# Kernel tuning notes

Hardware: AMD Instinct MI355X
Metric: run time of the kernel (lower is better)

Reference implementation:

```python
import jax, jax.numpy as jnp
import numpy as np

B, S, D, H = 2, 2048, 768, 12
DK = D // H


def setup_inputs() -> dict:
    key = jax.random.key(0)
    ks = jax.random.split(key, 12)
    inp = {
        "q": jax.random.normal(ks[0], (B, S, D), jnp.float32),
        "k": jax.random.normal(ks[1], (B, S, D), jnp.float32),
        "v": jax.random.normal(ks[2], (B, S, D), jnp.float32),
        # float mask: 1.0 where attention is disallowed (causal upper triangle)
        "mask": (1.0 - jnp.tril(jnp.ones((S, S), jnp.float32)))[None, None],
        "Wq": jax.random.normal(ks[3], (D, D), jnp.float32) / np.sqrt(D),
        "bq": jnp.zeros((D,), jnp.float32),
        "Wk": jax.random.normal(ks[4], (D, D), jnp.float32) / np.sqrt(D),
        "bk": jnp.zeros((D,), jnp.float32),
        "Wv": jax.random.normal(ks[5], (D, D), jnp.float32) / np.sqrt(D),
        "bv": jnp.zeros((D,), jnp.float32),
        "Wo": jax.random.normal(ks[6], (D, D), jnp.float32) / np.sqrt(D),
        "bo": jnp.zeros((D,), jnp.float32),
    }
    return inp


def _split_heads(x):
    # [B,S,D] -> [B,H,S,DK]
    b, s, _ = x.shape
    return x.reshape(b, s, H, DK).transpose(0, 2, 1, 3)


def reference(q, k, v, mask, Wq, bq, Wk, bk, Wv, bv, Wo, bo):
    Q = _split_heads(q @ Wq + bq)
    K = _split_heads(k @ Wk + bk)
    V = _split_heads(v @ Wv + bv)
    scale = jax.lax.rsqrt(jnp.float32(D))  # note: d_model, not d_k (faithful)
    logits = jnp.einsum("bhqd,bhkd->bhqk", Q, K) * scale
    logits = logits + (-1e9) * mask
    weights = jax.nn.softmax(logits, axis=-1)
    attn = jnp.einsum("bhqk,bhkd->bhqd", weights, V)
    attn = attn.transpose(0, 2, 1, 3).reshape(q.shape)  # [B,S,D]
    return jax.nn.relu(attn @ Wo + bo)
```

## Files before the change

### kernel.cpp

```cpp
#include <hip/hip_runtime.h>
#include <math.h>

#define BB 2
#define SS 2048
#define DD 768
#define HH 12
#define DKK 64
#define MM (BB*SS)

typedef _Float16 half_t;
using half8 = __attribute__((ext_vector_type(8))) _Float16;
using half4 = __attribute__((ext_vector_type(4))) _Float16;
using floatx4 = __attribute__((ext_vector_type(4))) float;

__global__ __launch_bounds__(256)
void prep(const float* __restrict__ q, const float* __restrict__ k,
          const float* __restrict__ v,
          const float* __restrict__ Wq, const float* __restrict__ Wk,
          const float* __restrict__ Wv, const float* __restrict__ Wo,
          half_t* __restrict__ qh, half_t* __restrict__ kh,
          half_t* __restrict__ vh,
          half_t* __restrict__ Wqt, half_t* __restrict__ Wkt,
          half_t* __restrict__ Wvt, half_t* __restrict__ Wot)
{
    __shared__ float tile[64][68];
    const int y = blockIdx.y;
    const int t = threadIdx.x;
    if (y < 3) {
        const float* src = y == 0 ? q : (y == 1 ? k : v);
        half_t* dst      = y == 0 ? qh : (y == 1 ? kh : vh);
        int i = blockIdx.x * 256 + t;
        float4 f = ((const float4*)src)[i];
        half4 hv;
        hv[0] = (half_t)f.x; hv[1] = (half_t)f.y;
        hv[2] = (half_t)f.z; hv[3] = (half_t)f.w;
        ((half4*)dst)[i] = hv;
    } else {
        int x = blockIdx.x;
        if (x >= 576) return;
        int w = x / 144, rem = x % 144;
        const float* W = w == 0 ? Wq : w == 1 ? Wk : w == 2 ? Wv : Wo;
        half_t* T      = w == 0 ? Wqt : w == 1 ? Wkt : w == 2 ? Wvt : Wot;
        int k0 = (rem % 12) * 64, n0 = (rem / 12) * 64;
        #pragma unroll
        for (int i = 0; i < 4; ++i) {
            int c = t + i * 256;
            int kr = c >> 4, nc = (c & 15) * 4;
            *(float4*)&tile[kr][nc] = *(const float4*)&W[(size_t)(k0 + kr) * DD + n0 + nc];
        }
        __syncthreads();
        #pragma unroll
        for (int i = 0; i < 4; ++i) {
            int c = t + i * 256;
            int nr = c >> 4, kc = (c & 15) * 4;
            half4 hv;
            #pragma unroll
            for (int jj = 0; jj < 4; ++jj) hv[jj] = (half_t)tile[kc + jj][nr];
            *(half4*)&T[(size_t)(n0 + nr) * DD + k0 + kc] = hv;
        }
    }
}

template<bool SWAP>
__device__ __forceinline__
void gemm_body(const half_t* __restrict__ A, const half_t* __restrict__ Bt,
               floatx4 (&acc)[4][2], half_t (*As)[72], half_t (*Bs)[72],
               int m0, int n0)
{
    const int t = threadIdx.x;
    const int lane = t & 63, wave = t >> 6;
    const int lr = lane & 15, lq = lane >> 4;
    const int wm = (wave >> 1) * 64, wn = (wave & 1) * 32;
    const int a_r = t >> 1,  a_c = (t & 1) * 32;
    const int b_r = t >> 2,  b_c = (t & 3) * 16;

    #pragma unroll
    for (int mi = 0; mi < 4; ++mi)
        #pragma unroll
        for (int ni = 0; ni < 2; ++ni)
            #pragma unroll
            for (int r = 0; r < 4; ++r) acc[mi][ni][r] = 0.f;

    for (int k0 = 0; k0 < DD; k0 += 64) {
        __syncthreads();
        #pragma unroll
        for (int jj = 0; jj < 4; ++jj)
            *(half8*)&As[a_r][a_c + jj * 8] =
                *(const half8*)&A[(size_t)(m0 + a_r) * DD + k0 + a_c + jj * 8];
        #pragma unroll
        for (int jj = 0; jj < 2; ++jj)
            *(half8*)&Bs[b_r][b_c + jj * 8] =
                *(const half8*)&Bt[(size_t)(n0 + b_r) * DD + k0 + b_c + jj * 8];
        __syncthreads();

        half8 af[4][2], bf[2][2];
        #pragma unroll
        for (int mi = 0; mi < 4; ++mi)
            #pragma unroll
            for (int kp = 0; kp < 2; ++kp)
                af[mi][kp] = *(const half8*)&As[wm + mi * 16 + lr][kp * 32 + lq * 8];
        #pragma unroll
        for (int ni = 0; ni < 2; ++ni)
            #pragma unroll
            for (int kp = 0; kp < 2; ++kp)
                bf[ni][kp] = *(const half8*)&Bs[wn + ni * 16 + lr][kp * 32 + lq * 8];

        #pragma unroll
        for (int mi = 0; mi < 4; ++mi)
            #pragma unroll
            for (int ni = 0; ni < 2; ++ni)
                #pragma unroll
                for (int kp = 0; kp < 2; ++kp) {
                    if (SWAP)
                        acc[mi][ni] = __builtin_amdgcn_mfma_f32_16x16x32_f16(
                            bf[ni][kp], af[mi][kp], acc[mi][ni], 0, 0, 0);
                    else
                        acc[mi][ni] = __builtin_amdgcn_mfma_f32_16x16x32_f16(
                            af[mi][kp], bf[ni][kp], acc[mi][ni], 0, 0, 0);
                }
    }
}

__global__ __launch_bounds__(256)
void proj_gemm(const half_t* __restrict__ qh, const half_t* __restrict__ kh,
               const half_t* __restrict__ vh,
               const half_t* __restrict__ Wqt, const half_t* __restrict__ Wkt,
               const half_t* __restrict__ Wvt,
               const float* __restrict__ bq, const float* __restrict__ bk,
               const float* __restrict__ bv,
               half_t* __restrict__ Qo, half_t* __restrict__ Ko,
               half_t* __restrict__ Vto)
{
    const int z = blockIdx.z;
    const half_t* A  = z == 0 ? qh  : z == 1 ? kh  : vh;
    const half_t* Bt = z == 0 ? Wqt : z == 1 ? Wkt : Wvt;
    const float* bias = z == 0 ? bq : z == 1 ? bk : bv;

    __shared__ half_t As[128][72];
    __shared__ half_t Bs[64][72];
    floatx4 acc[4][2];
    const int m0 = blockIdx.y * 128, n0 = blockIdx.x * 64;

    if (z == 2) gemm_body<true >(A, Bt, acc, As, Bs, m0, n0);
    else        gemm_body<false>(A, Bt, acc, As, Bs, m0, n0);

    const int lane = threadIdx.x & 63, wave = threadIdx.x >> 6;
    const int lr = lane & 15, lq = lane >> 4;
    const int wm = (wave >> 1) * 64, wn = (wave & 1) * 32;

    if (z == 2) {
        #pragma unroll
        for (int mi = 0; mi < 4; ++mi)
            #pragma unroll
            for (int ni = 0; ni < 2; ++ni)
                #pragma unroll
                for (int r = 0; r < 4; ++r) {
                    int dcol = n0 + wn + ni * 16 + lq * 4 + r;
                    int srow = m0 + wm + mi * 16 + lr;
                    int hh = dcol >> 6, d = dcol & 63;
                    int b2 = srow >> 11, sdx = srow & 2047;
                    Vto[((size_t)((b2 * HH + hh) * DKK + d)) * SS + sdx] =
                        (half_t)(acc[mi][ni][r] + bias[dcol]);
                }
    } else {
        const float sc = (z == 0) ? 0.03608439182435161f : 1.0f;
        half_t* O = z == 0 ? Qo : Ko;
        #pragma unroll
        for (int mi = 0; mi < 4; ++mi)
            #pragma unroll
            for (int ni = 0; ni < 2; ++ni)
                #pragma unroll
                for (int r = 0; r < 4; ++r) {
                    int row = m0 + wm + mi * 16 + lq * 4 + r;
                    int col = n0 + wn + ni * 16 + lr;
                    O[(size_t)row * DD + col] = (half_t)((acc[mi][ni][r] + bias[col]) * sc);
                }
    }
}

__global__ __launch_bounds__(256)
void out_gemm(const half_t* __restrict__ A, const half_t* __restrict__ Bt,
              const float* __restrict__ bias, float* __restrict__ C)
{
    __shared__ half_t As[128][72];
    __shared__ half_t Bs[64][72];
    floatx4 acc[4][2];
    const int m0 = blockIdx.y * 128, n0 = blockIdx.x * 64;
    gemm_body<false>(A, Bt, acc, As, Bs, m0, n0);

    const int lane = threadIdx.x & 63, wave = threadIdx.x >> 6;
    const int lr = lane & 15, lq = lane >> 4;
    const int wm = (wave >> 1) * 64, wn = (wave & 1) * 32;

    #pragma unroll
    for (int mi = 0; mi < 4; ++mi)
        #pragma unroll
        for (int ni = 0; ni < 2; ++ni)
            #pragma unroll
            for (int r = 0; r < 4; ++r) {
                int row = m0 + wm + mi * 16 + lq * 4 + r;
                int col = n0 + wn + ni * 16 + lr;
                C[(size_t)row * DD + col] = fmaxf(acc[mi][ni][r] + bias[col], 0.f);
            }
}

__global__ __launch_bounds__(256)
void attn_split(const half_t* __restrict__ Qf, const half_t* __restrict__ Kf,
                const half_t* __restrict__ Vt, half_t* __restrict__ Of,
                float* __restrict__ Opart, float* __restrict__ Lpart)
{
    __shared__ half_t Ks[64][72];
    __shared__ half_t Vs[64][72];
    __shared__ half_t Ps[4][32][72];

    const int i = blockIdx.x;
    const int bh = i % 24;
    const int j = i / 24;
    int qt, c; bool single;
    if (j < 8)       { qt = 15 - j;        c = 0; single = false; }
    else if (j < 16) { qt = 15 - (j - 8);  c = 1; single = false; }
    else             { qt = 7 - (j - 16);  c = 0; single = true;  }
    const int kt0 = c * 16;
    const int kt1 = (!single && c == 0) ? 16 : (2 * qt + 2);

    const int b = bh / HH, h = bh % HH;
    const int t = threadIdx.x;
    const int lane = t & 63, wave = t >> 6;
    const int lr = lane & 15, lq = lane >> 4;
    const int q0 = qt * 128;

    const int srow = t >> 3;
    const int scol = (t & 7) * 8;

    const half_t* Kbase = Kf + (size_t)(b * SS) * DD + h * DKK;
    const half_t* Vbase = Vt + (size_t)((b * HH + h) * DKK) * SS;

    half8 kpre[2], vpre[2];
    #pragma unroll
    for (int ii = 0; ii < 2; ++ii) {
        int row = srow + ii * 32;
        kpre[ii] = *(const half8*)&Kbase[(size_t)(kt0 * 64 + row) * DD + scol];
        vpre[ii] = *(const half8*)&Vbase[(size_t)row * SS + kt0 * 64 + scol];
    }

    half8 qa[2][2];
    #pragma unroll
    for (int qg = 0; qg < 2; ++qg) {
        const half_t* qptr =
            Qf + (size_t)(b * SS + q0 + wave * 32 + qg * 16 + lr) * DD + h * DKK;
        qa[qg][0] = *(const half8*)(qptr + lq * 8);
        qa[qg][1] = *(const half8*)(qptr + 32 + lq * 8);
    }

    floatx4 o[2][4];
    #pragma unroll
    for (int qg = 0; qg < 2; ++qg)
        #pragma unroll
        for (int nt = 0; nt < 4; ++nt)
            #pragma unroll
            for (int r = 0; r < 4; ++r) o[qg][nt][r] = 0.f;
    float l_run[2] = {0.f, 0.f};

    for (int kt = kt0; kt < kt1; ++kt) {
        __syncthreads();
        #pragma unroll
        for (int ii = 0; ii < 2; ++ii) {
            int row = srow + ii * 32;
            *(half8*)&Ks[row][scol] = kpre[ii];
            *(half8*)&Vs[row][scol] = vpre[ii];
        }
        __syncthreads();

        if (kt + 1 < kt1) {
            #pragma unroll
            for (int ii = 0; ii < 2; ++ii) {
                int row = srow + ii * 32;
                kpre[ii] = *(const half8*)&Kbase[(size_t)((kt + 1) * 64 + row) * DD + scol];
                vpre[ii] = *(const half8*)&Vbase[(size_t)row * SS + (kt + 1) * 64 + scol];
            }
        }

        floatx4 s[2][4];
        #pragma unroll
        for (int nt = 0; nt < 4; ++nt) {
            half8 kf0 = *(const half8*)&Ks[nt * 16 + lr][lq * 8];
            half8 kf1 = *(const half8*)&Ks[nt * 16 + lr][32 + lq * 8];
            #pragma unroll
            for (int qg = 0; qg < 2; ++qg) {
                floatx4 a = {0.f, 0.f, 0.f, 0.f};
                a = __builtin_amdgcn_mfma_f32_16x16x32_f16(kf0, qa[qg][0], a, 0, 0, 0);
                a = __builtin_amdgcn_mfma_f32_16x16x32_f16(kf1, qa[qg][1], a, 0, 0, 0);
                s[qg][nt] = a;
            }
        }

        if (kt >= 2 * qt) {
            #pragma unroll
            for (int qg = 0; qg < 2; ++qg) {
                int qrow = q0 + wave * 32 + qg * 16 + lr;
                #pragma unroll
                for (int nt = 0; nt < 4; ++nt)
                    #pragma unroll
                    for (int r = 0; r < 4; ++r) {
                        int key = kt * 64 + nt * 16 + lq * 4 + r;
                        if (key > qrow) s[qg][nt][r] = -1e30f;
                    }
            }
        }

        #pragma unroll
        for (int qg = 0; qg < 2; ++qg)
            #pragma unroll
            for (int nt = 0; nt < 4; ++nt) {
                half4 hp;
                #pragma unroll
                for (int r = 0; r < 4; ++r) {
                    float p = __expf(s[qg][nt][r]);
                    l_run[qg] += p;
                    hp[r] = (half_t)p;
                }
                *(half4*)&Ps[wave][qg * 16 + lr][nt * 16 + lq * 4] = hp;
            }

        __builtin_amdgcn_s_waitcnt(0xc07f);

        half8 pa[2][2];
        #pragma unroll
        for (int qg = 0; qg < 2; ++qg) {
            pa[qg][0] = *(const half8*)&Ps[wave][qg * 16 + lr][lq * 8];
            pa[qg][1] = *(const half8*)&Ps[wave][qg * 16 + lr][32 + lq * 8];
        }

        #pragma unroll
        for (int nt = 0; nt < 4; ++nt) {
            half8 vf0 = *(const half8*)&Vs[nt * 16 + lr][lq * 8];
            half8 vf1 = *(const half8*)&Vs[nt * 16 + lr][32 + lq * 8];
            #pragma unroll
            for (int qg = 0; qg < 2; ++qg) {
                o[qg][nt] = __builtin_amdgcn_mfma_f32_16x16x32_f16(vf0, pa[qg][0], o[qg][nt], 0, 0, 0);
                o[qg][nt] = __builtin_amdgcn_mfma_f32_16x16x32_f16(vf1, pa[qg][1], o[qg][nt], 0, 0, 0);
            }
        }
    }

    #pragma unroll
    for (int qg = 0; qg < 2; ++qg) {
        l_run[qg] += __shfl_xor(l_run[qg], 16);
        l_run[qg] += __shfl_xor(l_run[qg], 32);
    }

    if (single) {
        #pragma unroll
        for (int qg = 0; qg < 2; ++qg) {
            float inv = 1.f / l_run[qg];
            int qrow = q0 + wave * 32 + qg * 16 + lr;
            #pragma unroll
            for (int nt = 0; nt < 4; ++nt) {
                half4 hv;
                #pragma unroll
                for (int r = 0; r < 4; ++r) hv[r] = (half_t)(o[qg][nt][r] * inv);
                *(half4*)&Of[(size_t)(b * SS + qrow) * DD + h * DKK + nt * 16 + lq * 4] = hv;
            }
        }
    } else {
        const int p = (bh * 8 + (qt - 8)) * 2 + c;
        float* Ob = Opart + (size_t)p * 8192;
        #pragma unroll
        for (int qg = 0; qg < 2; ++qg) {
            int qq = wave * 32 + qg * 16 + lr;
            #pragma unroll
            for (int nt = 0; nt < 4; ++nt)
                *(floatx4*)&Ob[qq * 64 + nt * 16 + lq * 4] = o[qg][nt];
            if (lq == 0) Lpart[p * 128 + qq] = l_run[qg];
        }
    }
}

__global__ __launch_bounds__(256)
void attn_combine(const float* __restrict__ Opart, const float* __restrict__ Lpart,
                  half_t* __restrict__ Of)
{
    const int ib = blockIdx.x;
    const int bh = ib >> 3, qtm = ib & 7;
    const int b = bh / HH, h = bh % HH;
    const int p0 = (bh * 8 + qtm) * 2, p1 = p0 + 1;
    const int t = threadIdx.x;
    const int qq = t >> 1, ds0 = (t & 1) * 32;

    float inv = 1.f / (Lpart[p0 * 128 + qq] + Lpart[p1 * 128 + qq]);
    const float* O0 = Opart + (size_t)p0 * 8192 + qq * 64 + ds0;
    const float* O1 = Opart + (size_t)p1 * 8192 + qq * 64 + ds0;
    int srow = (qtm + 8) * 128 + qq;
    half_t* dst = Of + (size_t)(b * SS + srow) * DD + h * DKK + ds0;

    #pragma unroll
    for (int kk = 0; kk < 8; ++kk) {
        float4 a = *(const float4*)&O0[kk * 4];
        float4 c = *(const float4*)&O1[kk * 4];
        half4 hv;
        hv[0] = (half_t)((a.x + c.x) * inv);
        hv[1] = (half_t)((a.y + c.y) * inv);
        hv[2] = (half_t)((a.z + c.z) * inv);
        hv[3] = (half_t)((a.w + c.w) * inv);
        *(half4*)&dst[kk * 4] = hv;
    }
}

extern "C" void kernel_launch(void* const* d_in, const int* in_sizes, int n_in,
                              void* d_out, int out_size, void* d_ws, size_t ws_size,
                              hipStream_t stream)
{
    (void)in_sizes; (void)n_in; (void)out_size; (void)ws_size;
    const float* q  = (const float*)d_in[0];
    const float* k  = (const float*)d_in[1];
    const float* v  = (const float*)d_in[2];
    const float* Wq = (const float*)d_in[4];
    const float* bq = (const float*)d_in[5];
    const float* Wk = (const float*)d_in[6];
    const float* bk = (const float*)d_in[7];
    const float* Wv = (const float*)d_in[8];
    const float* bv = (const float*)d_in[9];
    const float* Wo = (const float*)d_in[10];
    const float* bo = (const float*)d_in[11];
    float* out = (float*)d_out;

    half_t* qh  = (half_t*)d_ws;
    half_t* kh  = qh  + (size_t)MM * DD;
    half_t* vh  = kh  + (size_t)MM * DD;
    half_t* Wqt = vh  + (size_t)MM * DD;
    half_t* Wkt = Wqt + (size_t)DD * DD;
    half_t* Wvt = Wkt + (size_t)DD * DD;
    half_t* Wot = Wvt + (size_t)DD * DD;
    half_t* Qo  = Wot + (size_t)DD * DD;
    half_t* Ko  = Qo  + (size_t)MM * DD;
    half_t* Vto = Ko  + (size_t)MM * DD;
    half_t* Ao  = Vto + (size_t)MM * DD;

    float* Opart = (float*)d_ws;
    float* Lpart = Opart + (size_t)384 * 8192;

    prep<<<dim3(3072, 4), 256, 0, stream>>>(q, k, v, Wq, Wk, Wv, Wo,
                                            qh, kh, vh, Wqt, Wkt, Wvt, Wot);
    proj_gemm<<<dim3(DD / 64, MM / 128, 3), 256, 0, stream>>>(
        qh, kh, vh, Wqt, Wkt, Wvt, bq, bk, bv, Qo, Ko, Vto);
    attn_split<<<dim3(24 * 24), 256, 0, stream>>>(Qo, Ko, Vto, Ao, Opart, Lpart);
    attn_combine<<<dim3(192), 256, 0, stream>>>(Opart, Lpart, Ao);
    out_gemm<<<dim3(DD / 64, MM / 128), 256, 0, stream>>>(Ao, Wot, bo, out);
}
```

Baseline: 205.8 us.

## Fuse input fp16 casts into projection GEMM, combine into out GEMM, double-buffer attention K/V

Drops the separate q/k/v fp32-to-fp16 conversion pass; the projection GEMM now loads fp32 activations and converts them while staging tiles in shared memory. The attn_combine kernel is removed and its split-KV merge (sum partials, divide by summed l) is folded into the output GEMM's A-tile load. Attention K/V shared tiles are double-buffered so one barrier per iteration is removed. The trade is twice the global bytes per A-tile load in the GEMMs, extra arithmetic repeated across the 12 column blocks of out_gemm, and more shared memory in attention.

```diff
diff --git a/kernel.cpp b/kernel.cpp
--- a/kernel.cpp
+++ b/kernel.cpp
@@ -14,58 +14,41 @@
 using floatx4 = __attribute__((ext_vector_type(4))) float;
 
 __global__ __launch_bounds__(256)
-void prep(const float* __restrict__ q, const float* __restrict__ k,
-          const float* __restrict__ v,
-          const float* __restrict__ Wq, const float* __restrict__ Wk,
+void prep(const float* __restrict__ Wq, const float* __restrict__ Wk,
           const float* __restrict__ Wv, const float* __restrict__ Wo,
-          half_t* __restrict__ qh, half_t* __restrict__ kh,
-          half_t* __restrict__ vh,
           half_t* __restrict__ Wqt, half_t* __restrict__ Wkt,
           half_t* __restrict__ Wvt, half_t* __restrict__ Wot)
 {
     __shared__ float tile[64][68];
-    const int y = blockIdx.y;
+    const int w = blockIdx.y;
+    const float* W = w == 0 ? Wq : w == 1 ? Wk : w == 2 ? Wv : Wo;
+    half_t* T      = w == 0 ? Wqt : w == 1 ? Wkt : w == 2 ? Wvt : Wot;
+    const int rem = blockIdx.x;
+    const int k0 = (rem % 12) * 64, n0 = (rem / 12) * 64;
     const int t = threadIdx.x;
-    if (y < 3) {
-        const float* src = y == 0 ? q : (y == 1 ? k : v);
-        half_t* dst      = y == 0 ? qh : (y == 1 ? kh : vh);
-        int i = blockIdx.x * 256 + t;
-        float4 f = ((const float4*)src)[i];
+    #pragma unroll
+    for (int i = 0; i < 4; ++i) {
+        int c = t + i * 256;
+        int kr = c >> 4, nc = (c & 15) * 4;
+        *(float4*)&tile[kr][nc] = *(const float4*)&W[(size_t)(k0 + kr) * DD + n0 + nc];
+    }
+    __syncthreads();
+    #pragma unroll
+    for (int i = 0; i < 4; ++i) {
+        int c = t + i * 256;
+        int nr = c >> 4, kc = (c & 15) * 4;
         half4 hv;
-        hv[0] = (half_t)f.x; hv[1] = (half_t)f.y;
-        hv[2] = (half_t)f.z; hv[3] = (half_t)f.w;
-        ((half4*)dst)[i] = hv;
-    } else {
-        int x = blockIdx.x;
-        if (x >= 576) return;
-        int w = x / 144, rem = x % 144;
-        const float* W = w == 0 ? Wq : w == 1 ? Wk : w == 2 ? Wv : Wo;
-        half_t* T      = w == 0 ? Wqt : w == 1 ? Wkt : w == 2 ? Wvt : Wot;
-        int k0 = (rem % 12) * 64, n0 = (rem / 12) * 64;
-        #pragma unroll
-        for (int i = 0; i < 4; ++i) {
-            int c = t + i * 256;
-            int kr = c >> 4, nc = (c & 15) * 4;
-            *(float4*)&tile[kr][nc] = *(const float4*)&W[(size_t)(k0 + kr) * DD + n0 + nc];
-        }
-        __syncthreads();
-        #pragma unroll
-        for (int i = 0; i < 4; ++i) {
-            int c = t + i * 256;
-            int nr = c >> 4, kc = (c & 15) * 4;
-            half4 hv;
-            #pragma unroll
-            for (int jj = 0; jj < 4; ++jj) hv[jj] = (half_t)tile[kc + jj][nr];
-            *(half4*)&T[(size_t)(n0 + nr) * DD + k0 + kc] = hv;
-        }
+        #pragma unroll
+        for (int jj = 0; jj < 4; ++jj) hv[jj] = (half_t)tile[kc + jj][nr];
+        *(half4*)&T[(size_t)(n0 + nr) * DD + k0 + kc] = hv;
     }
 }
 
 template<bool SWAP>
 __device__ __forceinline__
-void gemm_body(const half_t* __restrict__ A, const half_t* __restrict__ Bt,
-               floatx4 (&acc)[4][2], half_t (*As)[72], half_t (*Bs)[72],
-               int m0, int n0)
+void gemm_body_f32(const float* __restrict__ A, const half_t* __restrict__ Bt,
+                   floatx4 (&acc)[4][2], half_t (*As)[72], half_t (*Bs)[72],
+                   int m0, int n0)
 {
     const int t = threadIdx.x;
     const int lane = t & 63, wave = t >> 6;
@@ -84,9 +67,17 @@
     for (int k0 = 0; k0 < DD; k0 += 64) {
         __syncthreads();
         #pragma unroll
-        for (int jj = 0; jj < 4; ++jj)
-            *(half8*)&As[a_r][a_c + jj * 8] =
-                *(const half8*)&A[(size_t)(m0 + a_r) * DD + k0 + a_c + jj * 8];
+        for (int jj = 0; jj < 4; ++jj) {
+            const float* ap = &A[(size_t)(m0 + a_r) * DD + k0 + a_c + jj * 8];
+            float4 f0 = *(const float4*)ap;
+            float4 f1 = *(const float4*)(ap + 4);
+            half8 hv;
+            hv[0] = (half_t)f0.x; hv[1] = (half_t)f0.y;
+            hv[2] = (half_t)f0.z; hv[3] = (half_t)f0.w;
+            hv[4] = (half_t)f1.x; hv[5] = (half_t)f1.y;
+            hv[6] = (half_t)f1.z; hv[7] = (half_t)f1.w;
+            *(half8*)&As[a_r][a_c + jj * 8] = hv;
+        }
         #pragma unroll
         for (int jj = 0; jj < 2; ++jj)
             *(half8*)&Bs[b_r][b_c + jj * 8] =
@@ -122,8 +113,8 @@
 }
 
 __global__ __launch_bounds__(256)
-void proj_gemm(const half_t* __restrict__ qh, const half_t* __restrict__ kh,
-               const half_t* __restrict__ vh,
+void proj_gemm(const float* __restrict__ qf, const float* __restrict__ kf,
+               const float* __restrict__ vf,
                const half_t* __restrict__ Wqt, const half_t* __restrict__ Wkt,
                const half_t* __restrict__ Wvt,
                const float* __restrict__ bq, const float* __restrict__ bk,
@@ -132,7 +123,7 @@
                half_t* __restrict__ Vto)
 {
     const int z = blockIdx.z;
-    const half_t* A  = z == 0 ? qh  : z == 1 ? kh  : vh;
+    const float*  A  = z == 0 ? qf  : z == 1 ? kf  : vf;
     const half_t* Bt = z == 0 ? Wqt : z == 1 ? Wkt : Wvt;
     const float* bias = z == 0 ? bq : z == 1 ? bk : bv;
 
@@ -141,8 +132,8 @@
     floatx4 acc[4][2];
     const int m0 = blockIdx.y * 128, n0 = blockIdx.x * 64;
 
-    if (z == 2) gemm_body<true >(A, Bt, acc, As, Bs, m0, n0);
-    else        gemm_body<false>(A, Bt, acc, As, Bs, m0, n0);
+    if (z == 2) gemm_body_f32<true >(A, Bt, acc, As, Bs, m0, n0);
+    else        gemm_body_f32<false>(A, Bt, acc, As, Bs, m0, n0);
 
     const int lane = threadIdx.x & 63, wave = threadIdx.x >> 6;
     const int lr = lane & 15, lq = lane >> 4;
@@ -179,18 +170,101 @@
 }
 
 __global__ __launch_bounds__(256)
-void out_gemm(const half_t* __restrict__ A, const half_t* __restrict__ Bt,
+void out_gemm(const half_t* __restrict__ Ao, const float* __restrict__ Opart,
+              const float* __restrict__ Lpart, const half_t* __restrict__ Bt,
               const float* __restrict__ bias, float* __restrict__ C)
 {
     __shared__ half_t As[128][72];
     __shared__ half_t Bs[64][72];
-    floatx4 acc[4][2];
+    __shared__ float invl[HH][128];
+
+    const int t = threadIdx.x;
     const int m0 = blockIdx.y * 128, n0 = blockIdx.x * 64;
-    gemm_body<false>(A, Bt, acc, As, Bs, m0, n0);
-
-    const int lane = threadIdx.x & 63, wave = threadIdx.x >> 6;
+    const int bb = blockIdx.y >> 4;
+    const int qt = blockIdx.y & 15;
+    const bool split = (qt >= 8);
+
+    if (split) {
+        for (int idx = t; idx < HH * 128; idx += 256) {
+            int h = idx >> 7, qq = idx & 127;
+            int p0 = ((bb * HH + h) * 8 + (qt - 8)) * 2;
+            invl[h][qq] = 1.f / (Lpart[p0 * 128 + qq] + Lpart[(p0 + 1) * 128 + qq]);
+        }
+    }
+
+    const int lane = t & 63, wave = t >> 6;
     const int lr = lane & 15, lq = lane >> 4;
     const int wm = (wave >> 1) * 64, wn = (wave & 1) * 32;
+    const int a_r = t >> 1,  a_c = (t & 1) * 32;
+    const int b_r = t >> 2,  b_c = (t & 3) * 16;
+
+    floatx4 acc[4][2];
+    #pragma unroll
+    for (int mi = 0; mi < 4; ++mi)
+        #pragma unroll
+        for (int ni = 0; ni < 2; ++ni)
+            #pragma unroll
+            for (int r = 0; r < 4; ++r) acc[mi][ni][r] = 0.f;
+
+    for (int k0 = 0; k0 < DD; k0 += 64) {
+        __syncthreads();
+        if (!split) {
+            #pragma unroll
+            for (int jj = 0; jj < 4; ++jj)
+                *(half8*)&As[a_r][a_c + jj * 8] =
+                    *(const half8*)&Ao[(size_t)(m0 + a_r) * DD + k0 + a_c + jj * 8];
+        } else {
+            const int h = k0 >> 6;
+            const int p0 = ((bb * HH + h) * 8 + (qt - 8)) * 2;
+            const float* O0 = Opart + (size_t)p0 * 8192;
+            const float* O1 = O0 + 8192;
+            const float il = invl[h][a_r];
+            #pragma unroll
+            for (int jj = 0; jj < 4; ++jj) {
+                int d = a_c + jj * 8;
+                float4 x0 = *(const float4*)&O0[a_r * 64 + d];
+                float4 x1 = *(const float4*)&O0[a_r * 64 + d + 4];
+                float4 y0 = *(const float4*)&O1[a_r * 64 + d];
+                float4 y1 = *(const float4*)&O1[a_r * 64 + d + 4];
+                half8 hv;
+                hv[0] = (half_t)((x0.x + y0.x) * il);
+                hv[1] = (half_t)((x0.y + y0.y) * il);
+                hv[2] = (half_t)((x0.z + y0.z) * il);
+                hv[3] = (half_t)((x0.w + y0.w) * il);
+                hv[4] = (half_t)((x1.x + y1.x) * il);
+                hv[5] = (half_t)((x1.y + y1.y) * il);
+                hv[6] = (half_t)((x1.z + y1.z) * il);
+                hv[7] = (half_t)((x1.w + y1.w) * il);
+                *(half8*)&As[a_r][d] = hv;
+            }
+        }
+        #pragma unroll
+        for (int jj = 0; jj < 2; ++jj)
+            *(half8*)&Bs[b_r][b_c + jj * 8] =
+                *(const half8*)&Bt[(size_t)(n0 + b_r) * DD + k0 + b_c + jj * 8];
+        __syncthreads();
+
+        half8 af[4][2], bf[2][2];
+        #pragma unroll
+        for (int mi = 0; mi < 4; ++mi)
+            #pragma unroll
+            for (int kp = 0; kp < 2; ++kp)
+                af[mi][kp] = *(const half8*)&As[wm + mi * 16 + lr][kp * 32 + lq * 8];
+        #pragma unroll
+        for (int ni = 0; ni < 2; ++ni)
+            #pragma unroll
+            for (int kp = 0; kp < 2; ++kp)
+                bf[ni][kp] = *(const half8*)&Bs[wn + ni * 16 + lr][kp * 32 + lq * 8];
+
+        #pragma unroll
+        for (int mi = 0; mi < 4; ++mi)
+            #pragma unroll
+            for (int ni = 0; ni < 2; ++ni)
+                #pragma unroll
+                for (int kp = 0; kp < 2; ++kp)
+                    acc[mi][ni] = __builtin_amdgcn_mfma_f32_16x16x32_f16(
+                        af[mi][kp], bf[ni][kp], acc[mi][ni], 0, 0, 0);
+    }
 
     #pragma unroll
     for (int mi = 0; mi < 4; ++mi)
@@ -209,8 +283,8 @@
                 const half_t* __restrict__ Vt, half_t* __restrict__ Of,
                 float* __restrict__ Opart, float* __restrict__ Lpart)
 {
-    __shared__ half_t Ks[64][72];
-    __shared__ half_t Vs[64][72];
+    __shared__ half_t Ks[2][64][72];
+    __shared__ half_t Vs[2][64][72];
     __shared__ half_t Ps[4][32][72];
 
     const int i = blockIdx.x;
@@ -261,15 +335,16 @@
             for (int r = 0; r < 4; ++r) o[qg][nt][r] = 0.f;
     float l_run[2] = {0.f, 0.f};
 
+    #pragma unroll
+    for (int ii = 0; ii < 2; ++ii) {
+        int row = srow + ii * 32;
+        *(half8*)&Ks[0][row][scol] = kpre[ii];
+        *(half8*)&Vs[0][row][scol] = vpre[ii];
+    }
+    __syncthreads();
+
     for (int kt = kt0; kt < kt1; ++kt) {
-        __syncthreads();
-        #pragma unroll
-        for (int ii = 0; ii < 2; ++ii) {
-            int row = srow + ii * 32;
-            *(half8*)&Ks[row][scol] = kpre[ii];
-            *(half8*)&Vs[row][scol] = vpre[ii];
-        }
-        __syncthreads();
+        const int cur = (kt - kt0) & 1;
 
         if (kt + 1 < kt1) {
             #pragma unroll
@@ -283,8 +358,8 @@
         floatx4 s[2][4];
         #pragma unroll
         for (int nt = 0; nt < 4; ++nt) {
-            half8 kf0 = *(const half8*)&Ks[nt * 16 + lr][lq * 8];
-            half8 kf1 = *(const half8*)&Ks[nt * 16 + lr][32 + lq * 8];
+            half8 kf0 = *(const half8*)&Ks[cur][nt * 16 + lr][lq * 8];
+            half8 kf1 = *(const half8*)&Ks[cur][nt * 16 + lr][32 + lq * 8];
             #pragma unroll
             for (int qg = 0; qg < 2; ++qg) {
                 floatx4 a = {0.f, 0.f, 0.f, 0.f};
@@ -333,14 +408,24 @@
 
         #pragma unroll
         for (int nt = 0; nt < 4; ++nt) {
-            half8 vf0 = *(const half8*)&Vs[nt * 16 + lr][lq * 8];
-            half8 vf1 = *(const half8*)&Vs[nt * 16 + lr][32 + lq * 8];
+            half8 vf0 = *(const half8*)&Vs[cur][nt * 16 + lr][lq * 8];
+            half8 vf1 = *(const half8*)&Vs[cur][nt * 16 + lr][32 + lq * 8];
             #pragma unroll
             for (int qg = 0; qg < 2; ++qg) {
                 o[qg][nt] = __builtin_amdgcn_mfma_f32_16x16x32_f16(vf0, pa[qg][0], o[qg][nt], 0, 0, 0);
                 o[qg][nt] = __builtin_amdgcn_mfma_f32_16x16x32_f16(vf1, pa[qg][1], o[qg][nt], 0, 0, 0);
             }
         }
+
+        if (kt + 1 < kt1) {
+            #pragma unroll
+            for (int ii = 0; ii < 2; ++ii) {
+                int row = srow + ii * 32;
+                *(half8*)&Ks[cur ^ 1][row][scol] = kpre[ii];
+                *(half8*)&Vs[cur ^ 1][row][scol] = vpre[ii];
+            }
+        }
+        __syncthreads();
     }
 
     #pragma unroll
@@ -373,36 +458,6 @@
                 *(floatx4*)&Ob[qq * 64 + nt * 16 + lq * 4] = o[qg][nt];
             if (lq == 0) Lpart[p * 128 + qq] = l_run[qg];
         }
-    }
-}
-
-__global__ __launch_bounds__(256)
-void attn_combine(const float* __restrict__ Opart, const float* __restrict__ Lpart,
-                  half_t* __restrict__ Of)
-{
-    const int ib = blockIdx.x;
-    const int bh = ib >> 3, qtm = ib & 7;
-    const int b = bh / HH, h = bh % HH;
-    const int p0 = (bh * 8 + qtm) * 2, p1 = p0 + 1;
-    const int t = threadIdx.x;
-    const int qq = t >> 1, ds0 = (t & 1) * 32;
-
-    float inv = 1.f / (Lpart[p0 * 128 + qq] + Lpart[p1 * 128 + qq]);
-    const float* O0 = Opart + (size_t)p0 * 8192 + qq * 64 + ds0;
-    const float* O1 = Opart + (size_t)p1 * 8192 + qq * 64 + ds0;
-    int srow = (qtm + 8) * 128 + qq;
-    half_t* dst = Of + (size_t)(b * SS + srow) * DD + h * DKK + ds0;
-
-    #pragma unroll
-    for (int kk = 0; kk < 8; ++kk) {
-        float4 a = *(const float4*)&O0[kk * 4];
-        float4 c = *(const float4*)&O1[kk * 4];
-        half4 hv;
-        hv[0] = (half_t)((a.x + c.x) * inv);
-        hv[1] = (half_t)((a.y + c.y) * inv);
-        hv[2] = (half_t)((a.z + c.z) * inv);
-        hv[3] = (half_t)((a.w + c.w) * inv);
-        *(half4*)&dst[kk * 4] = hv;
     }
 }
 
@@ -424,10 +479,7 @@
     const float* bo = (const float*)d_in[11];
     float* out = (float*)d_out;
 
-    half_t* qh  = (half_t*)d_ws;
-    half_t* kh  = qh  + (size_t)MM * DD;
-    half_t* vh  = kh  + (size_t)MM * DD;
-    half_t* Wqt = vh  + (size_t)MM * DD;
+    half_t* Wqt = (half_t*)d_ws;
     half_t* Wkt = Wqt + (size_t)DD * DD;
     half_t* Wvt = Wkt + (size_t)DD * DD;
     half_t* Wot = Wvt + (size_t)DD * DD;
@@ -435,15 +487,12 @@
     half_t* Ko  = Qo  + (size_t)MM * DD;
     half_t* Vto = Ko  + (size_t)MM * DD;
     half_t* Ao  = Vto + (size_t)MM * DD;
-
-    float* Opart = (float*)d_ws;
+    float* Opart = (float*)(Ao + (size_t)MM * DD);
     float* Lpart = Opart + (size_t)384 * 8192;
 
-    prep<<<dim3(3072, 4), 256, 0, stream>>>(q, k, v, Wq, Wk, Wv, Wo,
-                                            qh, kh, vh, Wqt, Wkt, Wvt, Wot);
+    prep<<<dim3(144, 4), 256, 0, stream>>>(Wq, Wk, Wv, Wo, Wqt, Wkt, Wvt, Wot);
     proj_gemm<<<dim3(DD / 64, MM / 128, 3), 256, 0, stream>>>(
-        qh, kh, vh, Wqt, Wkt, Wvt, bq, bk, bv, Qo, Ko, Vto);
+        q, k, v, Wqt, Wkt, Wvt, bq, bk, bv, Qo, Ko, Vto);
     attn_split<<<dim3(24 * 24), 256, 0, stream>>>(Qo, Ko, Vto, Ao, Opart, Lpart);
-    attn_combine<<<dim3(192), 256, 0, stream>>>(Opart, Lpart, Ao);
-    out_gemm<<<dim3(DD / 64, MM / 128), 256, 0, stream>>>(Ao, Wot, bo, out);
-}
+    out_gemm<<<dim3(DD / 64, MM / 128), 256, 0, stream>>>(Ao, Opart, Lpart, Wot, bo, out);
+}
```

Result: slower. 285.1 us (+38.5%).

## Split causal attention KV range into finer chunks of eight tiles

Applied to the files above, without the earlier changes.

Replaces the two-way KV split for the upper query tiles with chunks of at most eight KV tiles, driven by lookup tables that assign (query tile, chunk) pairs to blocks ordered from heaviest to lightest. Query tiles 0-3 run as a single block, and the combine kernel now sums a variable number of partials. The intent is better load balance and more blocks across the GPU's compute units for the causal workload. In exchange it adds more partial-result traffic and more combine work, and the partial buffers move to a separate workspace region so they no longer alias the fp16 input buffers.

```diff
diff --git a/kernel.cpp b/kernel.cpp
--- a/kernel.cpp
+++ b/kernel.cpp
@@ -204,6 +204,13 @@
             }
 }
 
+__device__ const int QT_TAB[40] = {3,4,5,6,7,7,8,8,9,9,10,10,11,11,11,12,12,12,
+                                   13,13,13,14,14,14,15,15,15,15,
+                                   2,6,10,14, 1,5,9,13, 0,4,8,12};
+__device__ const int C_TAB[40]  = {0,0,0,0,0,1,0,1,0,1,0,1,0,1,2,0,1,2,
+                                   0,1,2,0,1,2,0,1,2,3,
+                                   0,1,2,3, 0,1,2,3, 0,1,2,3};
+
 __global__ __launch_bounds__(256)
 void attn_split(const half_t* __restrict__ Qf, const half_t* __restrict__ Kf,
                 const half_t* __restrict__ Vt, half_t* __restrict__ Of,
@@ -216,12 +223,12 @@
     const int i = blockIdx.x;
     const int bh = i % 24;
     const int j = i / 24;
-    int qt, c; bool single;
-    if (j < 8)       { qt = 15 - j;        c = 0; single = false; }
-    else if (j < 16) { qt = 15 - (j - 8);  c = 1; single = false; }
-    else             { qt = 7 - (j - 16);  c = 0; single = true;  }
-    const int kt0 = c * 16;
-    const int kt1 = (!single && c == 0) ? 16 : (2 * qt + 2);
+    const int qt = QT_TAB[j];
+    const int c  = C_TAB[j];
+    const bool single = (qt <= 3);
+    const int kt0 = c * 8;
+    const int iters = 2 * qt + 2;
+    const int kt1 = (kt0 + 8 < iters) ? (kt0 + 8) : iters;
 
     const int b = bh / HH, h = bh % HH;
     const int t = threadIdx.x;
@@ -363,7 +370,7 @@
             }
         }
     } else {
-        const int p = (bh * 8 + (qt - 8)) * 2 + c;
+        const int p = (bh * 12 + (qt - 4)) * 4 + c;
         float* Ob = Opart + (size_t)p * 8192;
         #pragma unroll
         for (int qg = 0; qg < 2; ++qg) {
@@ -381,27 +388,39 @@
                   half_t* __restrict__ Of)
 {
     const int ib = blockIdx.x;
-    const int bh = ib >> 3, qtm = ib & 7;
+    const int bh = ib / 12, qtm = ib % 12;
+    const int qt = qtm + 4;
+    const int nc = (2 * qt + 9) / 8;
     const int b = bh / HH, h = bh % HH;
-    const int p0 = (bh * 8 + qtm) * 2, p1 = p0 + 1;
+    const int pbase = (bh * 12 + qtm) * 4;
     const int t = threadIdx.x;
     const int qq = t >> 1, ds0 = (t & 1) * 32;
 
-    float inv = 1.f / (Lpart[p0 * 128 + qq] + Lpart[p1 * 128 + qq]);
-    const float* O0 = Opart + (size_t)p0 * 8192 + qq * 64 + ds0;
-    const float* O1 = Opart + (size_t)p1 * 8192 + qq * 64 + ds0;
-    int srow = (qtm + 8) * 128 + qq;
+    float l = 0.f;
+    for (int cc = 0; cc < nc; ++cc) l += Lpart[(pbase + cc) * 128 + qq];
+    const float inv = 1.f / l;
+
+    float4 acc[8];
+    #pragma unroll
+    for (int kk = 0; kk < 8; ++kk) acc[kk] = make_float4(0.f, 0.f, 0.f, 0.f);
+    for (int cc = 0; cc < nc; ++cc) {
+        const float* Ob = Opart + (size_t)(pbase + cc) * 8192 + qq * 64 + ds0;
+        #pragma unroll
+        for (int kk = 0; kk < 8; ++kk) {
+            float4 x = *(const float4*)&Ob[kk * 4];
+            acc[kk].x += x.x; acc[kk].y += x.y; acc[kk].z += x.z; acc[kk].w += x.w;
+        }
+    }
+
+    int srow = qt * 128 + qq;
     half_t* dst = Of + (size_t)(b * SS + srow) * DD + h * DKK + ds0;
-
     #pragma unroll
     for (int kk = 0; kk < 8; ++kk) {
-        float4 a = *(const float4*)&O0[kk * 4];
-        float4 c = *(const float4*)&O1[kk * 4];
         half4 hv;
-        hv[0] = (half_t)((a.x + c.x) * inv);
-        hv[1] = (half_t)((a.y + c.y) * inv);
-        hv[2] = (half_t)((a.z + c.z) * inv);
-        hv[3] = (half_t)((a.w + c.w) * inv);
+        hv[0] = (half_t)(acc[kk].x * inv);
+        hv[1] = (half_t)(acc[kk].y * inv);
+        hv[2] = (half_t)(acc[kk].z * inv);
+        hv[3] = (half_t)(acc[kk].w * inv);
         *(half4*)&dst[kk * 4] = hv;
     }
 }
@@ -435,15 +454,14 @@
     half_t* Ko  = Qo  + (size_t)MM * DD;
     half_t* Vto = Ko  + (size_t)MM * DD;
     half_t* Ao  = Vto + (size_t)MM * DD;
-
-    float* Opart = (float*)d_ws;
-    float* Lpart = Opart + (size_t)384 * 8192;
+    float* Opart = (float*)(Ao + (size_t)MM * DD);
+    float* Lpart = Opart + (size_t)1152 * 8192;
 
     prep<<<dim3(3072, 4), 256, 0, stream>>>(q, k, v, Wq, Wk, Wv, Wo,
                                             qh, kh, vh, Wqt, Wkt, Wvt, Wot);
     proj_gemm<<<dim3(DD / 64, MM / 128, 3), 256, 0, stream>>>(
         qh, kh, vh, Wqt, Wkt, Wvt, bq, bk, bv, Qo, Ko, Vto);
-    attn_split<<<dim3(24 * 24), 256, 0, stream>>>(Qo, Ko, Vto, Ao, Opart, Lpart);
-    attn_combine<<<dim3(192), 256, 0, stream>>>(Opart, Lpart, Ao);
+    attn_split<<<dim3(24 * 40), 256, 0, stream>>>(Qo, Ko, Vto, Ao, Opart, Lpart);
+    attn_combine<<<dim3(288), 256, 0, stream>>>(Opart, Lpart, Ao);
     out_gemm<<<dim3(DD / 64, MM / 128), 256, 0, stream>>>(Ao, Wot, bo, out);
 }
```

Result: no change. 209.7 us (+1.9%).
